# Kernel optimization log

Hardware: AMD Instinct MI355X
Metric: run time of the kernel (lower is better)

## Reference

```python
import jax, jax.numpy as jnp
import numpy as np

N_USERS = 4096
N_ITEMS = 4096
D = 64  # embedding_dim / out_features
N = N_USERS + N_ITEMS
ALPHA = 0.2  # LeakyReLU slope
NEG_INF = jnp.float32(-9e15)


def setup_inputs() -> dict:
    key = jax.random.key(0)
    ks = jax.random.split(key, 11)
    s = 0.05  # xavier-ish scale
    rn = lambda k, shape: jax.random.normal(k, shape, jnp.float32) * s
    adj = jax.random.randint(ks[0], (N, N), 0, 2, jnp.int32)
    return {
        "adj": adj,
        "user_emb": rn(ks[1], (N_USERS, D)),
        "item_emb": rn(ks[2], (N_ITEMS, D)),
        "W0_w": rn(ks[3], (D, D)), "W0_b": rn(ks[4], (D,)), "a0": rn(ks[5], (2 * D, 1)),
        "W1_w": rn(ks[6], (D, D)), "W1_b": rn(ks[7], (D,)), "a1": rn(ks[8], (2 * D, 1)),
        "out_w": rn(ks[9], (D, D)), "out_b": rn(ks[10], (D,)),
    }


def gat_layer(x, adj, W_w, W_b, a):
    # Wh: [N, D]
    Wh = x @ W_w.T + W_b
    # Original materializes [N,N,2D] concat then matmul with a.
    # Algebraically identical: e_ij = leakyrelu(a1 . Wh_i + a2 . Wh_j)
    src = Wh @ a[:D]          # [N, 1] -> row contribution
    dst = (Wh @ a[D:]).T      # [1, N] -> column contribution
    e = jax.nn.leaky_relu(src + dst, ALPHA)        # [N, N]
    e = jnp.where(adj > 0, e, NEG_INF)
    att = jax.nn.softmax(e, axis=1)                # dropout=0.0 (eval)
    return att @ Wh                                 # [N, D]


def reference(adj, user_emb, item_emb, W0_w, W0_b, a0, W1_w, W1_b, a1, out_w, out_b):
    x = jnp.concatenate([user_emb, item_emb], axis=0)  # [N, D]
    x = jax.nn.relu(gat_layer(x, adj, W0_w, W0_b, a0))
    x = jax.nn.relu(gat_layer(x, adj, W1_w, W1_b, a1))
    u, it = x[:N_USERS], x[N_USERS:]
    return (u @ out_w.T + out_b, it @ out_w.T + out_b)
```

## Files before the change

kernel.cpp:

```cpp
#include <hip/hip_runtime.h>


typedef __attribute__((ext_vector_type(8))) __bf16 bf16x8;
typedef __attribute__((ext_vector_type(4))) float  f32x4;

union Frag {
    bf16x8         v;
    unsigned int   w[4];
    unsigned short h[8];
};

__device__ __forceinline__ unsigned short f2bf(float f) {
    unsigned int u = __float_as_uint(f);
    u += 0x7FFFu + ((u >> 16) & 1u);
    return (unsigned short)(u >> 16);
}

__global__ __launch_bounds__(256) void k_prep(
    const float* __restrict__ ue, const float* __restrict__ ie,
    const float* __restrict__ num, const float* __restrict__ den, int mode,
    const float* __restrict__ W, const float* __restrict__ bias,
    const float* __restrict__ avec,
    unsigned short* __restrict__ WhT,
    float* __restrict__ sraw, float* __restrict__ draw)
{
    __shared__ float xs[64][65];
    __shared__ float Wt[64][65];
    __shared__ float sred[4][64];
    __shared__ float dred[4][64];

    int tid = threadIdx.x;
    int r0  = blockIdx.x * 64;

    for (int e = tid; e < 4096; e += 256) {
        int r = e >> 6, c = e & 63;
        int row = r0 + r;
        float v;
        if (mode) {
            float dd = fmaxf(den[row], 1e-20f);
            v = num[row * 64 + c] / dd;
            v = v > 0.f ? v : 0.f;
        } else {
            v = (row < 4096) ? ue[row * 64 + c] : ie[(row - 4096) * 64 + c];
        }
        xs[r][c] = v;
    }
    for (int e = tid; e < 4096; e += 256) {
        int o = e >> 6, c = e & 63;
        Wt[c][o] = W[e];
    }
    __syncthreads();

    int r = tid & 63, chunk = tid >> 6, c0 = chunk * 16;
    float acc[16];
#pragma unroll
    for (int o = 0; o < 16; o++) acc[o] = bias[c0 + o];
    for (int c = 0; c < 64; c++) {
        float xv = xs[r][c];
#pragma unroll
        for (int o = 0; o < 16; o++) acc[o] += xv * Wt[c][c0 + o];
    }

    float sp = 0.f, dp = 0.f;
#pragma unroll
    for (int o = 0; o < 16; o++) {
        sp += acc[o] * avec[c0 + o];
        dp += acc[o] * avec[64 + c0 + o];
    }
    sred[chunk][r] = sp;
    dred[chunk][r] = dp;

#pragma unroll
    for (int o = 0; o < 16; o++)
        WhT[(c0 + o) * 8192 + r0 + r] = f2bf(acc[o]);

    __syncthreads();
    if (tid < 64) {
        int g = r0 + tid;
        sraw[g] = sred[0][tid] + sred[1][tid] + sred[2][tid] + sred[3][tid];
        draw[g] = dred[0][tid] + dred[1][tid] + dred[2][tid] + dred[3][tid];
    }
}

__global__ __launch_bounds__(256) void k_agg(
    const int* __restrict__ adj, const unsigned short* __restrict__ WhT,
    const float* __restrict__ sraw, const float* __restrict__ draw,
    float* __restrict__ num, float* __restrict__ den)
{
    int tid  = threadIdx.x;
    int wave = tid >> 6, lane = tid & 63;
    int quad = lane >> 4, l16 = lane & 15;
    int rowblk = blockIdx.x, ks = blockIdx.y;
    int row = rowblk * 64 + wave * 16 + l16;
    const int KR = 1024;
    int k0 = ks * KR;

    float sv = sraw[row];

    f32x4 accs[4];
    f32x4 accd = {0.f, 0.f, 0.f, 0.f};
#pragma unroll
    for (int nt = 0; nt < 4; nt++) accs[nt] = accd;

    Frag ones;
    ones.w[0] = ones.w[1] = ones.w[2] = ones.w[3] = 0x3F803F80u;

    for (int kb = k0; kb < k0 + KR; kb += 32) {
        int kq = kb + quad * 8;

        const int4* ap = reinterpret_cast<const int4*>(adj + (size_t)row * 8192 + kq);
        int4 a0 = ap[0], a1 = ap[1];
        int ai[8] = {a0.x, a0.y, a0.z, a0.w, a1.x, a1.y, a1.z, a1.w};

        float4 dd0 = *reinterpret_cast<const float4*>(draw + kq);
        float4 dd1 = *reinterpret_cast<const float4*>(draw + kq + 4);
        float dv[8] = {dd0.x, dd0.y, dd0.z, dd0.w, dd1.x, dd1.y, dd1.z, dd1.w};

        Frag A;
#pragma unroll
        for (int j = 0; j < 8; j++) {
            float t  = sv + dv[j];
            float lr = t > 0.f ? t : 0.2f * t;
            float w  = (ai[j] != 0) ? __expf(lr) : 0.f;
            A.h[j] = f2bf(w);
        }

#pragma unroll
        for (int nt = 0; nt < 4; nt++) {
            Frag B;
            B.v = *reinterpret_cast<const bf16x8*>(WhT + (size_t)(nt * 16 + l16) * 8192 + kq);
            accs[nt] = __builtin_amdgcn_mfma_f32_16x16x32_bf16(A.v, B.v, accs[nt], 0, 0, 0);
        }
        accd = __builtin_amdgcn_mfma_f32_16x16x32_bf16(A.v, ones.v, accd, 0, 0, 0);
    }

    int rbase = rowblk * 64 + wave * 16 + quad * 4;
#pragma unroll
    for (int rr = 0; rr < 4; rr++) {
        if (l16 == 0) atomicAdd(den + rbase + rr, accd[rr]);
#pragma unroll
        for (int nt = 0; nt < 4; nt++)
            atomicAdd(num + (size_t)(rbase + rr) * 64 + nt * 16 + l16, accs[nt][rr]);
    }
}

__global__ __launch_bounds__(256) void k_out(
    const float* __restrict__ num, const float* __restrict__ den,
    const float* __restrict__ W, const float* __restrict__ bias,
    float* __restrict__ out)
{
    __shared__ float xs[64][65];
    __shared__ float Wt[64][65];
    int tid = threadIdx.x;
    int r0  = blockIdx.x * 64;

    for (int e = tid; e < 4096; e += 256) {
        int r = e >> 6, c = e & 63;
        float dd = fmaxf(den[r0 + r], 1e-20f);
        float v = num[(r0 + r) * 64 + c] / dd;
        xs[r][c] = v > 0.f ? v : 0.f;
    }
    for (int e = tid; e < 4096; e += 256) {
        int o = e >> 6, c = e & 63;
        Wt[c][o] = W[e];
    }
    __syncthreads();

    int r = tid & 63, chunk = tid >> 6, c0 = chunk * 16;
    float acc[16];
#pragma unroll
    for (int o = 0; o < 16; o++) acc[o] = bias[c0 + o];
    for (int c = 0; c < 64; c++) {
        float xv = xs[r][c];
#pragma unroll
        for (int o = 0; o < 16; o++) acc[o] += xv * Wt[c][c0 + o];
    }
#pragma unroll
    for (int o = 0; o < 16; o++)
        out[(r0 + r) * 64 + c0 + o] = acc[o];
}

extern "C" void kernel_launch(void* const* d_in, const int* in_sizes, int n_in,
                              void* d_out, int out_size, void* d_ws, size_t ws_size,
                              hipStream_t stream)
{
    const int*   adj = (const int*)d_in[0];
    const float* ue  = (const float*)d_in[1];
    const float* ie  = (const float*)d_in[2];
    const float* W0w = (const float*)d_in[3];
    const float* W0b = (const float*)d_in[4];
    const float* a0  = (const float*)d_in[5];
    const float* W1w = (const float*)d_in[6];
    const float* W1b = (const float*)d_in[7];
    const float* a1  = (const float*)d_in[8];
    const float* Ow  = (const float*)d_in[9];
    const float* Ob  = (const float*)d_in[10];

    char* ws = (char*)d_ws;
    size_t off = 0;
    auto alloc = [&](size_t bytes) -> char* {
        char* p = ws + off;
        off += (bytes + 255) & ~(size_t)255;
        return p;
    };
    unsigned short* WhT0 = (unsigned short*)alloc(64 * 8192 * 2);
    unsigned short* WhT1 = (unsigned short*)alloc(64 * 8192 * 2);
    float* sr0  = (float*)alloc(8192 * 4);
    float* dr0  = (float*)alloc(8192 * 4);
    float* sr1  = (float*)alloc(8192 * 4);
    float* dr1  = (float*)alloc(8192 * 4);
    float* num0 = (float*)alloc(8192 * 64 * 4);
    float* den0 = (float*)alloc(8192 * 4);
    float* num1 = (float*)alloc(8192 * 64 * 4);
    float* den1 = (float*)alloc(8192 * 4);

    hipMemsetAsync(num0, 0, (8192 * 64 + 8192) * 4, stream);
    hipMemsetAsync(num1, 0, (8192 * 64 + 8192) * 4, stream);

    k_prep<<<128, 256, 0, stream>>>(ue, ie, (const float*)nullptr, (const float*)nullptr, 0,
                                    W0w, W0b, a0, WhT0, sr0, dr0);
    k_agg<<<dim3(128, 8), 256, 0, stream>>>(adj, WhT0, sr0, dr0, num0, den0);
    k_prep<<<128, 256, 0, stream>>>(ue, ie, num0, den0, 1,
                                    W1w, W1b, a1, WhT1, sr1, dr1);
    k_agg<<<dim3(128, 8), 256, 0, stream>>>(adj, WhT1, sr1, dr1, num1, den1);
    k_out<<<128, 256, 0, stream>>>(num1, den1, Ow, Ob, (float*)d_out);
}
```

Before: 583.1 us.

## Bit-pack adjacency in first layer and replace atomics with split partial buffers

The first aggregation pass reads the int32 adjacency and writes a bit-packed copy, so the second layer reads 8 MB of bits instead of 256 MB of ints. Atomic accumulation of numerator and denominator is replaced by per-split partial buffers that the next kernel sums, which also removes the memsets. The split counts change to 16 for layer 0 and 8 for layer 1, and occupancy hints are added. The cost is extra partial-buffer traffic and a byte-granular scattered write of the bitmask in layer 0.

```diff
diff --git a/kernel.cpp b/kernel.cpp
--- a/kernel.cpp
+++ b/kernel.cpp
@@ -16,9 +16,52 @@
     return (unsigned short)(u >> 16);
 }
 
-__global__ __launch_bounds__(256) void k_prep(
+__device__ __forceinline__ void prep_tail(
+    float (*xs)[65], float (*Wt)[65], float (*sred)[64], float (*dred)[64],
+    const float* __restrict__ W, const float* __restrict__ bias,
+    const float* __restrict__ avec,
+    unsigned short* __restrict__ WhT, float* __restrict__ sraw,
+    float* __restrict__ draw, int tid, int r0)
+{
+    for (int e = tid; e < 4096; e += 256) {
+        int o = e >> 6, c = e & 63;
+        Wt[c][o] = W[e];
+    }
+    __syncthreads();
+
+    int r = tid & 63, chunk = tid >> 6, c0 = chunk * 16;
+    float acc[16];
+#pragma unroll
+    for (int o = 0; o < 16; o++) acc[o] = bias[c0 + o];
+    for (int c = 0; c < 64; c++) {
+        float xv = xs[r][c];
+#pragma unroll
+        for (int o = 0; o < 16; o++) acc[o] += xv * Wt[c][c0 + o];
+    }
+
+    float sp = 0.f, dp = 0.f;
+#pragma unroll
+    for (int o = 0; o < 16; o++) {
+        sp += acc[o] * avec[c0 + o];
+        dp += acc[o] * avec[64 + c0 + o];
+    }
+    sred[chunk][r] = sp;
+    dred[chunk][r] = dp;
+
+#pragma unroll
+    for (int o = 0; o < 16; o++)
+        WhT[(c0 + o) * 8192 + r0 + r] = f2bf(acc[o]);
+
+    __syncthreads();
+    if (tid < 64) {
+        int g = r0 + tid;
+        sraw[g] = sred[0][tid] + sred[1][tid] + sred[2][tid] + sred[3][tid];
+        draw[g] = dred[0][tid] + dred[1][tid] + dred[2][tid] + dred[3][tid];
+    }
+}
+
+__global__ __launch_bounds__(256) void k_prep0(
     const float* __restrict__ ue, const float* __restrict__ ie,
-    const float* __restrict__ num, const float* __restrict__ den, int mode,
     const float* __restrict__ W, const float* __restrict__ bias,
     const float* __restrict__ avec,
     unsigned short* __restrict__ WhT,
@@ -28,72 +71,64 @@
     __shared__ float Wt[64][65];
     __shared__ float sred[4][64];
     __shared__ float dred[4][64];
-
-    int tid = threadIdx.x;
-    int r0  = blockIdx.x * 64;
+    int tid = threadIdx.x, r0 = blockIdx.x * 64;
 
     for (int e = tid; e < 4096; e += 256) {
         int r = e >> 6, c = e & 63;
         int row = r0 + r;
-        float v;
-        if (mode) {
-            float dd = fmaxf(den[row], 1e-20f);
-            v = num[row * 64 + c] / dd;
-            v = v > 0.f ? v : 0.f;
-        } else {
-            v = (row < 4096) ? ue[row * 64 + c] : ie[(row - 4096) * 64 + c];
-        }
-        xs[r][c] = v;
-    }
-    for (int e = tid; e < 4096; e += 256) {
-        int o = e >> 6, c = e & 63;
-        Wt[c][o] = W[e];
-    }
-    __syncthreads();
-
-    int r = tid & 63, chunk = tid >> 6, c0 = chunk * 16;
-    float acc[16];
-#pragma unroll
-    for (int o = 0; o < 16; o++) acc[o] = bias[c0 + o];
-    for (int c = 0; c < 64; c++) {
-        float xv = xs[r][c];
-#pragma unroll
-        for (int o = 0; o < 16; o++) acc[o] += xv * Wt[c][c0 + o];
-    }
-
-    float sp = 0.f, dp = 0.f;
-#pragma unroll
-    for (int o = 0; o < 16; o++) {
-        sp += acc[o] * avec[c0 + o];
-        dp += acc[o] * avec[64 + c0 + o];
-    }
-    sred[chunk][r] = sp;
-    dred[chunk][r] = dp;
-
-#pragma unroll
-    for (int o = 0; o < 16; o++)
-        WhT[(c0 + o) * 8192 + r0 + r] = f2bf(acc[o]);
-
-    __syncthreads();
+        xs[r][c] = (row < 4096) ? ue[row * 64 + c] : ie[(row - 4096) * 64 + c];
+    }
+    prep_tail(xs, Wt, sred, dred, W, bias, avec, WhT, sraw, draw, tid, r0);
+}
+
+template <int NS>
+__global__ __launch_bounds__(256) void k_prep1(
+    const float* __restrict__ numP, const float* __restrict__ denP,
+    const float* __restrict__ W, const float* __restrict__ bias,
+    const float* __restrict__ avec,
+    unsigned short* __restrict__ WhT,
+    float* __restrict__ sraw, float* __restrict__ draw)
+{
+    __shared__ float xs[64][65];
+    __shared__ float Wt[64][65];
+    __shared__ float sred[4][64];
+    __shared__ float dred[4][64];
+    __shared__ float dtot[64];
+    int tid = threadIdx.x, r0 = blockIdx.x * 64;
+
     if (tid < 64) {
-        int g = r0 + tid;
-        sraw[g] = sred[0][tid] + sred[1][tid] + sred[2][tid] + sred[3][tid];
-        draw[g] = dred[0][tid] + dred[1][tid] + dred[2][tid] + dred[3][tid];
-    }
-}
-
-__global__ __launch_bounds__(256) void k_agg(
-    const int* __restrict__ adj, const unsigned short* __restrict__ WhT,
+        float s = 0.f;
+#pragma unroll
+        for (int p = 0; p < NS; p++) s += denP[p * 8192 + r0 + tid];
+        dtot[tid] = fmaxf(s, 1e-20f);
+    }
+    __syncthreads();
+    for (int e = tid; e < 4096; e += 256) {
+        int r = e >> 6, c = e & 63;
+        float s = 0.f;
+#pragma unroll
+        for (int p = 0; p < NS; p++)
+            s += numP[(size_t)p * 524288 + (r0 + r) * 64 + c];
+        float v = s / dtot[r];
+        xs[r][c] = v > 0.f ? v : 0.f;
+    }
+    prep_tail(xs, Wt, sred, dred, W, bias, avec, WhT, sraw, draw, tid, r0);
+}
+
+template <int RAW, int NSPLIT>
+__global__ __launch_bounds__(256, 8) void k_agg(
+    const int* __restrict__ adj, unsigned int* __restrict__ adjbits,
+    const unsigned short* __restrict__ WhT,
     const float* __restrict__ sraw, const float* __restrict__ draw,
-    float* __restrict__ num, float* __restrict__ den)
-{
+    float* __restrict__ numP, float* __restrict__ denP)
+{
+    const int KR = 8192 / NSPLIT;
     int tid  = threadIdx.x;
     int wave = tid >> 6, lane = tid & 63;
     int quad = lane >> 4, l16 = lane & 15;
     int rowblk = blockIdx.x, ks = blockIdx.y;
     int row = rowblk * 64 + wave * 16 + l16;
-    const int KR = 1024;
-    int k0 = ks * KR;
+    int k0  = ks * KR;
 
     float sv = sraw[row];
 
@@ -108,9 +143,21 @@
     for (int kb = k0; kb < k0 + KR; kb += 32) {
         int kq = kb + quad * 8;
 
-        const int4* ap = reinterpret_cast<const int4*>(adj + (size_t)row * 8192 + kq);
-        int4 a0 = ap[0], a1 = ap[1];
-        int ai[8] = {a0.x, a0.y, a0.z, a0.w, a1.x, a1.y, a1.z, a1.w};
+        unsigned int mask8;
+        if constexpr (RAW) {
+            const int4* ap = reinterpret_cast<const int4*>(adj + (size_t)row * 8192 + kq);
+            int4 a0 = ap[0], a1 = ap[1];
+            int ai[8] = {a0.x, a0.y, a0.z, a0.w, a1.x, a1.y, a1.z, a1.w};
+            mask8 = 0;
+#pragma unroll
+            for (int j = 0; j < 8; j++)
+                if (ai[j] != 0) mask8 |= (1u << j);
+            reinterpret_cast<unsigned char*>(adjbits)[(size_t)row * 1024 + (kb >> 3) + quad] =
+                (unsigned char)mask8;
+        } else {
+            unsigned int word = adjbits[row * 256 + (kb >> 5)];
+            mask8 = (word >> (quad * 8)) & 0xFFu;
+        }
 
         float4 dd0 = *reinterpret_cast<const float4*>(draw + kq);
         float4 dd1 = *reinterpret_cast<const float4*>(draw + kq + 4);
@@ -121,7 +168,7 @@
         for (int j = 0; j < 8; j++) {
             float t  = sv + dv[j];
             float lr = t > 0.f ? t : 0.2f * t;
-            float w  = (ai[j] != 0) ? __expf(lr) : 0.f;
+            float w  = ((mask8 >> j) & 1u) ? __expf(lr) : 0.f;
             A.h[j] = f2bf(w);
         }
 
@@ -135,29 +182,41 @@
     }
 
     int rbase = rowblk * 64 + wave * 16 + quad * 4;
+    size_t nb = (size_t)ks * 524288;
 #pragma unroll
     for (int rr = 0; rr < 4; rr++) {
-        if (l16 == 0) atomicAdd(den + rbase + rr, accd[rr]);
+        if (l16 == 0) denP[ks * 8192 + rbase + rr] = accd[rr];
 #pragma unroll
         for (int nt = 0; nt < 4; nt++)
-            atomicAdd(num + (size_t)(rbase + rr) * 64 + nt * 16 + l16, accs[nt][rr]);
-    }
-}
-
+            numP[nb + (size_t)(rbase + rr) * 64 + nt * 16 + l16] = accs[nt][rr];
+    }
+}
+
+template <int NS>
 __global__ __launch_bounds__(256) void k_out(
-    const float* __restrict__ num, const float* __restrict__ den,
+    const float* __restrict__ numP, const float* __restrict__ denP,
     const float* __restrict__ W, const float* __restrict__ bias,
     float* __restrict__ out)
 {
     __shared__ float xs[64][65];
     __shared__ float Wt[64][65];
-    int tid = threadIdx.x;
-    int r0  = blockIdx.x * 64;
-
+    __shared__ float dtot[64];
+    int tid = threadIdx.x, r0 = blockIdx.x * 64;
+
+    if (tid < 64) {
+        float s = 0.f;
+#pragma unroll
+        for (int p = 0; p < NS; p++) s += denP[p * 8192 + r0 + tid];
+        dtot[tid] = fmaxf(s, 1e-20f);
+    }
+    __syncthreads();
     for (int e = tid; e < 4096; e += 256) {
         int r = e >> 6, c = e & 63;
-        float dd = fmaxf(den[r0 + r], 1e-20f);
-        float v = num[(r0 + r) * 64 + c] / dd;
+        float s = 0.f;
+#pragma unroll
+        for (int p = 0; p < NS; p++)
+            s += numP[(size_t)p * 524288 + (r0 + r) * 64 + c];
+        float v = s / dtot[r];
         xs[r][c] = v > 0.f ? v : 0.f;
     }
     for (int e = tid; e < 4096; e += 256) {
@@ -196,6 +255,8 @@
     const float* Ow  = (const float*)d_in[9];
     const float* Ob  = (const float*)d_in[10];
 
+    constexpr int NS0 = 16, NS1 = 8;
+
     char* ws = (char*)d_ws;
     size_t off = 0;
     auto alloc = [&](size_t bytes) -> char* {
@@ -203,25 +264,21 @@
         off += (bytes + 255) & ~(size_t)255;
         return p;
     };
-    unsigned short* WhT0 = (unsigned short*)alloc(64 * 8192 * 2);
-    unsigned short* WhT1 = (unsigned short*)alloc(64 * 8192 * 2);
-    float* sr0  = (float*)alloc(8192 * 4);
-    float* dr0  = (float*)alloc(8192 * 4);
-    float* sr1  = (float*)alloc(8192 * 4);
-    float* dr1  = (float*)alloc(8192 * 4);
-    float* num0 = (float*)alloc(8192 * 64 * 4);
-    float* den0 = (float*)alloc(8192 * 4);
-    float* num1 = (float*)alloc(8192 * 64 * 4);
-    float* den1 = (float*)alloc(8192 * 4);
-
-    hipMemsetAsync(num0, 0, (8192 * 64 + 8192) * 4, stream);
-    hipMemsetAsync(num1, 0, (8192 * 64 + 8192) * 4, stream);
-
-    k_prep<<<128, 256, 0, stream>>>(ue, ie, (const float*)nullptr, (const float*)nullptr, 0,
-                                    W0w, W0b, a0, WhT0, sr0, dr0);
-    k_agg<<<dim3(128, 8), 256, 0, stream>>>(adj, WhT0, sr0, dr0, num0, den0);
-    k_prep<<<128, 256, 0, stream>>>(ue, ie, num0, den0, 1,
-                                    W1w, W1b, a1, WhT1, sr1, dr1);
-    k_agg<<<dim3(128, 8), 256, 0, stream>>>(adj, WhT1, sr1, dr1, num1, den1);
-    k_out<<<128, 256, 0, stream>>>(num1, den1, Ow, Ob, (float*)d_out);
-}
+    float*          numP    = (float*)alloc((size_t)NS0 * 524288 * 4);
+    float*          denP    = (float*)alloc((size_t)NS0 * 8192 * 4);
+    unsigned int*   adjbits = (unsigned int*)alloc(8192 * 1024);
+    unsigned short* WhT0    = (unsigned short*)alloc(64 * 8192 * 2);
+    unsigned short* WhT1    = (unsigned short*)alloc(64 * 8192 * 2);
+    float* sr0 = (float*)alloc(8192 * 4);
+    float* dr0 = (float*)alloc(8192 * 4);
+    float* sr1 = (float*)alloc(8192 * 4);
+    float* dr1 = (float*)alloc(8192 * 4);
+
+    k_prep0<<<128, 256, 0, stream>>>(ue, ie, W0w, W0b, a0, WhT0, sr0, dr0);
+    k_agg<1, NS0><<<dim3(128, NS0), 256, 0, stream>>>(adj, adjbits, WhT0,
+                                                      sr0, dr0, numP, denP);
+    k_prep1<NS0><<<128, 256, 0, stream>>>(numP, denP, W1w, W1b, a1, WhT1, sr1, dr1);
+    k_agg<0, NS1><<<dim3(128, NS1), 256, 0, stream>>>((const int*)nullptr, adjbits, WhT1,
+                                                      sr1, dr1, numP, denP);
+    k_out<NS1><<<128, 256, 0, stream>>>(numP, denP, Ow, Ob, (float*)d_out);
+}
```

New measurement: 573.1 us. About the same (-1.7%).
